# Kernel tuning notes

Measured on AMD Instinct MI355X. Metric: run time of the kernel, lower is better.

The kernel has to match this reference:

```python
import jax, jax.numpy as jnp
import numpy as np

N, K, DIN = 2, 2048, 1024
H, DOUT = 16, 64


def setup_inputs() -> dict:
    key = jax.random.key(0)
    ks = jax.random.split(key, 12)
    c_qk = float(np.sqrt(6.0 / (DIN + DOUT)))  # per-head q/k init scale
    c_v = c_qk  # dim_q == dim_v == DOUT here
    u = lambda k, shape, c: jax.random.uniform(k, shape, jnp.float32, -c, c)
    inp = {
        "query": jax.random.normal(ks[0], (N, K, DIN), jnp.float32),
        "key": jax.random.normal(ks[1], (N, K, DIN), jnp.float32),
        "value": jax.random.normal(ks[2], (N, K, DIN), jnp.float32),
        "mask": jax.random.randint(ks[3], (N, K, K), 0, 2) > 0,  # bool (N,K,K)
        # stacked per-head projection weights: (H, DIN, DOUT), biases (H, DOUT)
        "Wq": u(ks[4], (H, DIN, DOUT), c_qk),
        "bq": u(ks[5], (H, DOUT), c_qk),
        "Wk": u(ks[6], (H, DIN, DOUT), c_qk),
        "bk": u(ks[7], (H, DOUT), c_qk),
        "Wv": u(ks[8], (H, DIN, DOUT), c_v),
        "bv": u(ks[9], (H, DOUT), c_v),
        # output projection: (H*DOUT, DIN)
        "Wp": u(ks[10], (H * DOUT, DIN), c_qk),
        "bp": u(ks[11], (DIN,), c_qk),
    }
    return inp


def reference(query, key, value, mask, Wq, bq, Wk, bk, Wv, bv, Wp, bp):
    # Per-head projections, batched over heads: (N,K,DIN) x (H,DIN,DOUT) -> (N,H,K,DOUT)
    q = jnp.einsum("nkm,hmd->nhkd", query, Wq) + bq[None, :, None, :]
    k = jnp.einsum("nkm,hmd->nhkd", key, Wk) + bk[None, :, None, :]
    v = jnp.einsum("nkm,hmd->nhkd", value, Wv) + bv[None, :, None, :]
    # scaled dot-product scores: (N,H,K,K), scaled by sqrt(per-head dim)
    scores = jnp.einsum("nhkd,nhld->nhkl", q, k) / jnp.sqrt(jnp.asarray(DOUT, q.dtype))
    scores = jnp.where(mask[:, None, :, :], jnp.asarray(-1e9, scores.dtype), scores)
    w = jax.nn.softmax(scores, axis=-1)
    y = jnp.einsum("nhkl,nhld->nhkd", w, v)  # (N,H,K,DOUT)
    # concat heads along feature dim (head order matches torch cat over head list)
    y = jnp.transpose(y, (0, 2, 1, 3)).reshape(N, K, H * DOUT)
    return y @ Wp + bp
```

## Files before the change

kernel.cpp:

```cpp
#include <hip/hip_runtime.h>
#include <hip/hip_bf16.h>

typedef __attribute__((ext_vector_type(8))) __bf16 bf16x8;
typedef __attribute__((ext_vector_type(4))) float floatx4;

#define NB 2
#define SEQ 2048
#define DIN 1024
#define NH 16
#define DH 64
#define DMODEL 1024
#define BQ 128
#define BK 64
#define PAD 72
#define QSCALE 0.18033688011112042f

__device__ __forceinline__ float bf2f(unsigned short u) {
    return __uint_as_float(((unsigned)u) << 16);
}
__device__ __forceinline__ unsigned short f2bf(float f) {
    unsigned u = __float_as_uint(f);
    unsigned r = (u + 0x7FFFu + ((u >> 16) & 1u)) >> 16;
    return (unsigned short)r;
}
__device__ __forceinline__ float ldin(const void* p, size_t idx, int isbf) {
    return isbf ? bf2f(((const unsigned short*)p)[idx]) : ((const float*)p)[idx];
}

__device__ __forceinline__ int wave_is_bf16(const void* p) {
    unsigned short u = ((const unsigned short*)p)[2 * (threadIdx.x & 63)];
    int e = (u >> 7) & 0xFF;
    int sane = (u == 0 || (e > 100 && e < 140)) ? 1 : 0;
    return __popcll(__ballot(sane)) >= 32;
}
__device__ __forceinline__ int wave_mask_is_int(const void* p) {
    int v = ((const int*)p)[threadIdx.x & 63];
    int zo = (v == 0 || v == 1) ? 1 : 0;
    return __popcll(__ballot(zo)) >= 48;
}

__global__ __launch_bounds__(256) void prep(
    const void* __restrict__ q, const void* __restrict__ k, const void* __restrict__ v,
    const void* __restrict__ mask,
    const void* __restrict__ wq, const void* __restrict__ wk,
    const void* __restrict__ wv, const void* __restrict__ wp,
    unsigned short* __restrict__ a0, unsigned short* __restrict__ a1,
    unsigned short* __restrict__ a2,
    unsigned short* __restrict__ t0, unsigned short* __restrict__ t1,
    unsigned short* __restrict__ t2, unsigned short* __restrict__ t3,
    unsigned int* __restrict__ mbits)
{
    __shared__ float xls[64][68];
    const int b = blockIdx.x;
    const int tid = threadIdx.x;
    if (b < 12288) {
        int z = b >> 12, blk = b & 4095;
        const void* src = (z == 0) ? q : (z == 1) ? k : v;
        unsigned short* dst = (z == 0) ? a0 : (z == 1) ? a1 : a2;
        int isbf = wave_is_bf16(src);
        size_t i = ((size_t)blk * 256 + tid) * 4;
        if (isbf) {
            *(ushort4*)&dst[i] = *(const ushort4*)((const unsigned short*)src + i);
        } else {
            float4 f = *(const float4*)((const float*)src + i);
            ushort4 o;
            o.x = f2bf(f.x); o.y = f2bf(f.y); o.z = f2bf(f.z); o.w = f2bf(f.w);
            *(ushort4*)&dst[i] = o;
        }
    } else if (b < 13312) {
        int blk = b - 12288;
        int w = blk * 256 + tid;
        int is_int = wave_mask_is_int(mask);
        unsigned bits = 0;
        if (is_int) {
            const int4* p = (const int4*)mask + (size_t)w * 8;
#pragma unroll
            for (int g = 0; g < 8; ++g) {
                int4 vv = p[g];
                bits |= (unsigned)(vv.x != 0) << (g * 4 + 0);
                bits |= (unsigned)(vv.y != 0) << (g * 4 + 1);
                bits |= (unsigned)(vv.z != 0) << (g * 4 + 2);
                bits |= (unsigned)(vv.w != 0) << (g * 4 + 3);
            }
        } else {
            const uint4* p = (const uint4*)mask + (size_t)w * 2;
#pragma unroll
            for (int g = 0; g < 2; ++g) {
                uint4 vv = p[g];
                unsigned ws4[4] = {vv.x, vv.y, vv.z, vv.w};
#pragma unroll
                for (int c = 0; c < 4; ++c)
#pragma unroll
                    for (int bb = 0; bb < 4; ++bb)
                        bits |= (unsigned)(((ws4[c] >> (8 * bb)) & 0xFFu) != 0)
                                << (g * 16 + c * 4 + bb);
            }
        }
        mbits[w] = bits;
    } else {
        int zb = b - 13312;
        int z = zb >> 8, t = zb & 255;
        const void* src = (z == 0) ? wq : (z == 1) ? wk : (z == 2) ? wv : wp;
        unsigned short* dst = (z == 0) ? t0 : (z == 1) ? t1 : (z == 2) ? t2 : t3;
        int isbf = wave_is_bf16(src);
        int r = tid >> 2, cs = (tid & 3) * 16;
        if (z < 3) {
            int h = t >> 4, m0 = (t & 15) * 64;
#pragma unroll
            for (int j = 0; j < 16; ++j)
                xls[r][cs + j] = ldin(src, (size_t)h * 65536 + (size_t)(m0 + r) * 64 + cs + j, isbf);
            __syncthreads();
            int d2 = tid >> 2, ms = (tid & 3) * 16;
            size_t orow = (size_t)(h * 64 + d2) * 1024 + m0 + ms;
#pragma unroll
            for (int g = 0; g < 4; ++g) {
                ushort4 o;
                o.x = f2bf(xls[ms + g * 4 + 0][d2]);
                o.y = f2bf(xls[ms + g * 4 + 1][d2]);
                o.z = f2bf(xls[ms + g * 4 + 2][d2]);
                o.w = f2bf(xls[ms + g * 4 + 3][d2]);
                *(ushort4*)&dst[orow + g * 4] = o;
            }
        } else {
            int m0 = (t >> 4) * 64, c0 = (t & 15) * 64;
#pragma unroll
            for (int j = 0; j < 16; ++j)
                xls[r][cs + j] = ldin(src, (size_t)(m0 + r) * 1024 + c0 + cs + j, isbf);
            __syncthreads();
            int d2 = tid >> 2, ms = (tid & 3) * 16;
            size_t orow = (size_t)(c0 + d2) * 1024 + m0 + ms;
#pragma unroll
            for (int g = 0; g < 4; ++g) {
                ushort4 o;
                o.x = f2bf(xls[ms + g * 4 + 0][d2]);
                o.y = f2bf(xls[ms + g * 4 + 1][d2]);
                o.z = f2bf(xls[ms + g * 4 + 2][d2]);
                o.w = f2bf(xls[ms + g * 4 + 3][d2]);
                *(ushort4*)&dst[orow + g * 4] = o;
            }
        }
    }
}

__global__ __launch_bounds__(256) void gemm_mfma(
    const unsigned short* __restrict__ A0, const unsigned short* __restrict__ A1,
    const unsigned short* __restrict__ A2,
    const unsigned short* __restrict__ B0, const unsigned short* __restrict__ B1,
    const unsigned short* __restrict__ B2,
    const void* __restrict__ bias0, const void* __restrict__ bias1,
    const void* __restrict__ bias2,
    void* __restrict__ C0, void* __restrict__ C1, void* __restrict__ C2,
    int mode0)
{
    const int z = blockIdx.z;
    const unsigned short* A  = (z == 0) ? A0 : (z == 1) ? A1 : A2;
    const unsigned short* BT = (z == 0) ? B0 : (z == 1) ? B1 : B2;
    const void* bias = (z == 0) ? bias0 : (z == 1) ? bias1 : bias2;
    void* C = (z == 0) ? C0 : (z == 1) ? C1 : C2;
    const int mode = mode0 + z;
    const int isbf = wave_is_bf16(bias);
    const float scl = (mode == 0) ? QSCALE : 1.0f;

    const int n0  = blockIdx.x * 128;
    const int m0g = blockIdx.y * 128;
    const int tid = threadIdx.x;
    const int wave = tid >> 6, lane = tid & 63;
    const int l16 = lane & 15, quad = lane >> 4;
    const int wm = wave & 1, wn = wave >> 1;

    __shared__ __align__(16) unsigned short smem[17408];
    unsigned short* As = smem;
    unsigned short* Bs = smem + 8192;

    floatx4 acc[4][4];
#pragma unroll
    for (int mt = 0; mt < 4; ++mt)
#pragma unroll
        for (int nt = 0; nt < 4; ++nt) acc[mt][nt] = floatx4{0.f, 0.f, 0.f, 0.f};

    for (int kk = 0; kk < 1024; kk += 64) {
#pragma unroll
        for (int j = 0; j < 4; ++j) {
            int i = tid + j * 256;
            int row = i >> 3, seg = (i & 7) * 8;
            *(bf16x8*)&As[row * 64 + seg] = *(const bf16x8*)&A[(size_t)(m0g + row) * 1024 + kk + seg];
            *(bf16x8*)&Bs[row * 64 + seg] = *(const bf16x8*)&BT[(size_t)(n0 + row) * 1024 + kk + seg];
        }
        __syncthreads();
#pragma unroll
        for (int ks = 0; ks < 2; ++ks) {
            bf16x8 af[4], bf[4];
#pragma unroll
            for (int mt = 0; mt < 4; ++mt)
                af[mt] = *(const bf16x8*)&As[(wm * 64 + mt * 16 + l16) * 64 + ks * 32 + quad * 8];
#pragma unroll
            for (int nt = 0; nt < 4; ++nt)
                bf[nt] = *(const bf16x8*)&Bs[(wn * 64 + nt * 16 + l16) * 64 + ks * 32 + quad * 8];
#pragma unroll
            for (int mt = 0; mt < 4; ++mt)
#pragma unroll
                for (int nt = 0; nt < 4; ++nt)
                    acc[mt][nt] = __builtin_amdgcn_mfma_f32_16x16x32_bf16(af[mt], bf[nt], acc[mt][nt], 0, 0, 0);
        }
        __syncthreads();
    }

    float bv4[4];
#pragma unroll
    for (int nt = 0; nt < 4; ++nt)
        bv4[nt] = ldin(bias, n0 + wn * 64 + nt * 16 + l16, isbf);

    if (mode <= 1) {
        unsigned short* O = (unsigned short*)C;
#pragma unroll
        for (int mt = 0; mt < 4; ++mt)
#pragma unroll
            for (int reg = 0; reg < 4; ++reg) {
                int row = m0g + wm * 64 + mt * 16 + quad * 4 + reg;
                int nb = row >> 11, kq = row & (SEQ - 1);
#pragma unroll
                for (int nt = 0; nt < 4; ++nt) {
                    int c = n0 + wn * 64 + nt * 16 + l16;
                    int h = c >> 6, d = c & 63;
                    O[(((size_t)nb * NH + h) * SEQ + kq) * DH + d] =
                        f2bf((acc[mt][nt][reg] + bv4[nt]) * scl);
                }
            }
    } else if (mode == 2) {
#pragma unroll
        for (int mt = 0; mt < 4; ++mt)
#pragma unroll
            for (int nt = 0; nt < 4; ++nt)
#pragma unroll
                for (int reg = 0; reg < 4; ++reg) {
                    int m_l = wm * 64 + mt * 16 + quad * 4 + reg;
                    int c_l = wn * 64 + nt * 16 + l16;
                    smem[c_l * 136 + m_l] = f2bf(acc[mt][nt][reg] + bv4[nt]);
                }
        __syncthreads();
        unsigned short* O = (unsigned short*)C;
        int nb = m0g >> 11;
        int kq0 = m0g & (SEQ - 1);
#pragma unroll
        for (int j = 0; j < 8; ++j) {
            int i = tid + j * 256;
            int c_l = i >> 4, m8 = (i & 15) * 8;
            int cg = n0 + c_l, h = cg >> 6, d = cg & 63;
            *(bf16x8*)&O[(((size_t)nb * NH + h) * DH + d) * SEQ + kq0 + m8] =
                *(const bf16x8*)&smem[c_l * 136 + m8];
        }
    } else {
        unsigned short* Ob = (unsigned short*)C;
        float* Of = (float*)C;
#pragma unroll
        for (int mt = 0; mt < 4; ++mt)
#pragma unroll
            for (int reg = 0; reg < 4; ++reg) {
                int row = m0g + wm * 64 + mt * 16 + quad * 4 + reg;
#pragma unroll
                for (int nt = 0; nt < 4; ++nt) {
                    int c = n0 + wn * 64 + nt * 16 + l16;
                    float v = acc[mt][nt][reg] + bv4[nt];
                    if (isbf) Ob[(size_t)row * DMODEL + c] = f2bf(v);
                    else      Of[(size_t)row * DMODEL + c] = v;
                }
            }
    }
}

__global__ __launch_bounds__(256) void attn_mfma(
    const unsigned short* __restrict__ qws, const unsigned short* __restrict__ kws,
    const unsigned short* __restrict__ vtws, const unsigned int* __restrict__ mbits,
    unsigned short* __restrict__ yws)
{
    const int qt   = blockIdx.x;
    const int h    = blockIdx.y;
    const int n    = blockIdx.z;
    const int tid  = threadIdx.x;
    const int wave = tid >> 6;
    const int lane = tid & 63;
    const int l16  = lane & 15;
    const int quad = lane >> 4;

    __shared__ __align__(16) unsigned short Ks[2][BK * PAD];
    __shared__ __align__(16) unsigned short VTs[2][DH * PAD];
    __shared__ __align__(16) unsigned short Ps[4][32 * PAD];
    __shared__ unsigned int Ms[2][BQ][2];

    const size_t base_nh = ((size_t)n * NH + h) * SEQ * DH;
    const size_t base_vt = ((size_t)n * NH + h) * DH * SEQ;
    const int q0 = qt * BQ;
    const unsigned int* mrow_base = mbits + ((size_t)n * SEQ + q0) * (SEQ / 32);

    const int srow = tid >> 3, sseg = (tid & 7) * 8;
    const int mr = tid >> 1, mw = tid & 1;

    bf16x8 af[2][2];
#pragma unroll
    for (int mt = 0; mt < 2; ++mt) {
        const unsigned short* qp =
            qws + base_nh + (size_t)(q0 + wave * 32 + mt * 16 + l16) * DH + quad * 8;
        af[mt][0] = *(const bf16x8*)qp;
        af[mt][1] = *(const bf16x8*)(qp + 32);
    }

    {
#pragma unroll
        for (int j = 0; j < 2; ++j) {
            int row = srow + j * 32;
            *(bf16x8*)&Ks[0][row * PAD + sseg] =
                *(const bf16x8*)&kws[base_nh + (size_t)row * DH + sseg];
            *(bf16x8*)&VTs[0][row * PAD + sseg] =
                *(const bf16x8*)&vtws[base_vt + (size_t)row * SEQ + sseg];
        }
        Ms[0][mr][mw] = mrow_base[(size_t)mr * (SEQ / 32) + mw];
    }

    floatx4 O[2][4];
#pragma unroll
    for (int mt = 0; mt < 2; ++mt)
#pragma unroll
        for (int dt = 0; dt < 4; ++dt) O[mt][dt] = floatx4{0.f, 0.f, 0.f, 0.f};
    float lrow[2][4] = {};

    __syncthreads();

    for (int it = 0; it < SEQ / BK; ++it) {
        const int cur = it & 1;
        const bool has_next = (it + 1) < (SEQ / BK);
        const int j0n = (it + 1) * BK;

        bf16x8 nk[2], nv[2];
        unsigned int nm = 0;
        if (has_next) {
#pragma unroll
            for (int j = 0; j < 2; ++j) {
                int row = srow + j * 32;
                nk[j] = *(const bf16x8*)&kws[base_nh + (size_t)(j0n + row) * DH + sseg];
                nv[j] = *(const bf16x8*)&vtws[base_vt + (size_t)row * SEQ + j0n + sseg];
            }
            nm = mrow_base[(size_t)mr * (SEQ / 32) + (j0n >> 5) + mw];
        }

        bf16x8 bfK[4][2];
#pragma unroll
        for (int nt = 0; nt < 4; ++nt)
#pragma unroll
            for (int ks = 0; ks < 2; ++ks)
                bfK[nt][ks] = *(const bf16x8*)&Ks[cur][(nt * 16 + l16) * PAD + ks * 32 + quad * 8];

        float S[2][4][4];
#pragma unroll
        for (int mt = 0; mt < 2; ++mt)
#pragma unroll
            for (int nt = 0; nt < 4; ++nt) {
                floatx4 c = {0.f, 0.f, 0.f, 0.f};
                c = __builtin_amdgcn_mfma_f32_16x16x32_bf16(af[mt][0], bfK[nt][0], c, 0, 0, 0);
                c = __builtin_amdgcn_mfma_f32_16x16x32_bf16(af[mt][1], bfK[nt][1], c, 0, 0, 0);
                S[mt][nt][0] = c[0]; S[mt][nt][1] = c[1];
                S[mt][nt][2] = c[2]; S[mt][nt][3] = c[3];
            }

#pragma unroll
        for (int mt = 0; mt < 2; ++mt)
#pragma unroll
            for (int r = 0; r < 4; ++r) {
                int lrowi = wave * 32 + mt * 16 + quad * 4 + r;
                unsigned wlo = Ms[cur][lrowi][0], whi = Ms[cur][lrowi][1];
#pragma unroll
                for (int nt = 0; nt < 4; ++nt) {
                    unsigned w = (nt & 2) ? whi : wlo;
                    int bit = (w >> ((nt & 1) * 16 + l16)) & 1;
                    float s = bit ? -1e9f : S[mt][nt][r];
                    float p = exp2f(s);
                    lrow[mt][r] += p;
                    Ps[wave][(mt * 16 + quad * 4 + r) * PAD + nt * 16 + l16] =
                        (unsigned short)(__float_as_uint(p) >> 16);
                }
            }

        bf16x8 pa[2][2], vb[4][2];
#pragma unroll
        for (int mt = 0; mt < 2; ++mt)
#pragma unroll
            for (int ks = 0; ks < 2; ++ks)
                pa[mt][ks] = *(const bf16x8*)&Ps[wave][(mt * 16 + l16) * PAD + ks * 32 + quad * 8];
#pragma unroll
        for (int dt = 0; dt < 4; ++dt)
#pragma unroll
            for (int ks = 0; ks < 2; ++ks)
                vb[dt][ks] = *(const bf16x8*)&VTs[cur][(dt * 16 + l16) * PAD + ks * 32 + quad * 8];
#pragma unroll
        for (int mt = 0; mt < 2; ++mt)
#pragma unroll
            for (int dt = 0; dt < 4; ++dt) {
                O[mt][dt] = __builtin_amdgcn_mfma_f32_16x16x32_bf16(pa[mt][0], vb[dt][0], O[mt][dt], 0, 0, 0);
                O[mt][dt] = __builtin_amdgcn_mfma_f32_16x16x32_bf16(pa[mt][1], vb[dt][1], O[mt][dt], 0, 0, 0);
            }

        if (has_next) {
            const int nxt = cur ^ 1;
#pragma unroll
            for (int j = 0; j < 2; ++j) {
                int row = srow + j * 32;
                *(bf16x8*)&Ks[nxt][row * PAD + sseg] = nk[j];
                *(bf16x8*)&VTs[nxt][row * PAD + sseg] = nv[j];
            }
            Ms[nxt][mr][mw] = nm;
        }
        __syncthreads();
    }

#pragma unroll
    for (int mt = 0; mt < 2; ++mt)
#pragma unroll
        for (int r = 0; r < 4; ++r)
            for (int o = 1; o < 16; o <<= 1) lrow[mt][r] += __shfl_xor(lrow[mt][r], o);

#pragma unroll
    for (int mt = 0; mt < 2; ++mt)
#pragma unroll
        for (int r = 0; r < 4; ++r) {
            int row = q0 + wave * 32 + mt * 16 + quad * 4 + r;
            float l = lrow[mt][r];
            float inv = (l > 0.f) ? 1.f / l : 0.f;
#pragma unroll
            for (int dt = 0; dt < 4; ++dt) {
                int col = h * DH + dt * 16 + l16;
                yws[((size_t)n * SEQ + row) * DMODEL + col] = f2bf(O[mt][dt][r] * inv);
            }
        }
}

extern "C" void kernel_launch(void* const* d_in, const int* in_sizes, int n_in,
                              void* d_out, int out_size, void* d_ws, size_t ws_size,
                              hipStream_t stream) {
    const void* query = d_in[0];
    const void* key_  = d_in[1];
    const void* value = d_in[2];
    const void* mask  = d_in[3];
    const void* Wq = d_in[4];
    const void* bq = d_in[5];
    const void* Wk = d_in[6];
    const void* bk = d_in[7];
    const void* Wv = d_in[8];
    const void* bv = d_in[9];
    const void* Wp = d_in[10];
    const void* bp = d_in[11];

    const size_t per = (size_t)NB * NH * SEQ * DH;
    unsigned short* us = (unsigned short*)d_ws;
    unsigned short* qws  = us;
    unsigned short* kws  = us + per;
    unsigned short* vtws = us + 2 * per;
    unsigned short* abf0 = us + 3 * per;
    unsigned short* abf1 = us + 4 * per;
    unsigned short* abf2 = us + 5 * per;
    unsigned short* wt0  = us + 6 * per;
    unsigned short* wt1  = wt0 + 1048576;
    unsigned short* wt2  = wt1 + 1048576;
    unsigned short* wt3  = wt2 + 1048576;
    unsigned int* mbits  = (unsigned int*)(wt3 + 1048576);
    unsigned short* yws = abf0;

    prep<<<dim3(14336), 256, 0, stream>>>(query, key_, value, mask,
                                          Wq, Wk, Wv, Wp,
                                          abf0, abf1, abf2,
                                          wt0, wt1, wt2, wt3, mbits);
    gemm_mfma<<<dim3(8, 32, 3), 256, 0, stream>>>(abf0, abf1, abf2, wt0, wt1, wt2,
                                                  bq, bk, bv, qws, kws, vtws, 0);
    attn_mfma<<<dim3(SEQ / BQ, NH, NB), 256, 0, stream>>>(qws, kws, vtws, mbits, yws);
    gemm_mfma<<<dim3(8, 32, 1), 256, 0, stream>>>(yws, yws, yws, wt3, wt3, wt3,
                                                  bp, bp, bp, d_out, d_out, d_out, 3);
}
```

Measured before the change: 311.3 us.

## Use direct global-to-LDS loads with XOR swizzle in GEMM and attention

```diff
diff --git a/kernel.cpp b/kernel.cpp
--- a/kernel.cpp
+++ b/kernel.cpp
@@ -1,5 +1,6 @@
 #include <hip/hip_runtime.h>
 #include <hip/hip_bf16.h>
+#include <stdint.h>
 
 typedef __attribute__((ext_vector_type(8))) __bf16 bf16x8;
 typedef __attribute__((ext_vector_type(4))) float floatx4;
@@ -25,6 +26,15 @@
 }
 __device__ __forceinline__ float ldin(const void* p, size_t idx, int isbf) {
     return isbf ? bf2f(((const unsigned short*)p)[idx]) : ((const float*)p)[idx];
+}
+
+__device__ __forceinline__ void gl_lds16(const void* g, void* l) {
+    __builtin_amdgcn_global_load_lds(
+        reinterpret_cast<__attribute__((address_space(1))) unsigned int*>(
+            reinterpret_cast<uintptr_t>(g)),
+        reinterpret_cast<__attribute__((address_space(3))) unsigned int*>(
+            reinterpret_cast<uintptr_t>(l)),
+        16, 0, 0);
 }
 
 __device__ __forceinline__ int wave_is_bf16(const void* p) {
@@ -178,13 +188,15 @@
 #pragma unroll
         for (int nt = 0; nt < 4; ++nt) acc[mt][nt] = floatx4{0.f, 0.f, 0.f, 0.f};
 
+    const int lrow8 = lane >> 3;
+    const int lseg  = (lane & 7) * 8;
+
     for (int kk = 0; kk < 1024; kk += 64) {
 #pragma unroll
         for (int j = 0; j < 4; ++j) {
-            int i = tid + j * 256;
-            int row = i >> 3, seg = (i & 7) * 8;
-            *(bf16x8*)&As[row * 64 + seg] = *(const bf16x8*)&A[(size_t)(m0g + row) * 1024 + kk + seg];
-            *(bf16x8*)&Bs[row * 64 + seg] = *(const bf16x8*)&BT[(size_t)(n0 + row) * 1024 + kk + seg];
+            int row0 = wave * 8 + j * 32;
+            gl_lds16(&A[(size_t)(m0g + row0 + lrow8) * 1024 + kk + lseg], &As[row0 * 64]);
+            gl_lds16(&BT[(size_t)(n0 + row0 + lrow8) * 1024 + kk + lseg], &Bs[row0 * 64]);
         }
         __syncthreads();
 #pragma unroll
@@ -282,8 +294,8 @@
     const int l16  = lane & 15;
     const int quad = lane >> 4;
 
-    __shared__ __align__(16) unsigned short Ks[2][BK * PAD];
-    __shared__ __align__(16) unsigned short VTs[2][DH * PAD];
+    __shared__ __align__(16) unsigned short Ks[2][BK * DH];
+    __shared__ __align__(16) unsigned short VTs[2][DH * BK];
     __shared__ __align__(16) unsigned short Ps[4][32 * PAD];
     __shared__ unsigned int Ms[2][BQ][2];
 
@@ -292,8 +304,17 @@
     const int q0 = qt * BQ;
     const unsigned int* mrow_base = mbits + ((size_t)n * SEQ + q0) * (SEQ / 32);
 
-    const int srow = tid >> 3, sseg = (tid & 7) * 8;
+    const int srow8  = lane >> 3;
+    const int schunk = ((lane & 7) ^ srow8) * 8;
     const int mr = tid >> 1, mw = tid & 1;
+
+    const int swz = l16 & 7;
+    int koff[2], voff[2];
+#pragma unroll
+    for (int ks = 0; ks < 2; ++ks) {
+        koff[ks] = l16 * DH + (((ks * 4 + quad) ^ swz) * 8);
+        voff[ks] = l16 * BK + (((ks * 4 + quad) ^ swz) * 8);
+    }
 
     bf16x8 af[2][2];
 #pragma unroll
@@ -306,12 +327,10 @@
 
     {
 #pragma unroll
-        for (int j = 0; j < 2; ++j) {
-            int row = srow + j * 32;
-            *(bf16x8*)&Ks[0][row * PAD + sseg] =
-                *(const bf16x8*)&kws[base_nh + (size_t)row * DH + sseg];
-            *(bf16x8*)&VTs[0][row * PAD + sseg] =
-                *(const bf16x8*)&vtws[base_vt + (size_t)row * SEQ + sseg];
+        for (int c = 0; c < 2; ++c) {
+            int rl = wave * 16 + c * 8;
+            gl_lds16(&kws[base_nh + (size_t)(rl + srow8) * DH + schunk], &Ks[0][rl * DH]);
+            gl_lds16(&vtws[base_vt + (size_t)(rl + srow8) * SEQ + schunk], &VTs[0][rl * BK]);
         }
         Ms[0][mr][mw] = mrow_base[(size_t)mr * (SEQ / 32) + mw];
     }
@@ -326,18 +345,17 @@
     __syncthreads();
 
     for (int it = 0; it < SEQ / BK; ++it) {
-        const int cur = it & 1;
+        const int cur = it & 1, nxt = cur ^ 1;
         const bool has_next = (it + 1) < (SEQ / BK);
         const int j0n = (it + 1) * BK;
 
-        bf16x8 nk[2], nv[2];
         unsigned int nm = 0;
         if (has_next) {
 #pragma unroll
-            for (int j = 0; j < 2; ++j) {
-                int row = srow + j * 32;
-                nk[j] = *(const bf16x8*)&kws[base_nh + (size_t)(j0n + row) * DH + sseg];
-                nv[j] = *(const bf16x8*)&vtws[base_vt + (size_t)row * SEQ + j0n + sseg];
+            for (int c = 0; c < 2; ++c) {
+                int rl = wave * 16 + c * 8;
+                gl_lds16(&kws[base_nh + (size_t)(j0n + rl + srow8) * DH + schunk], &Ks[nxt][rl * DH]);
+                gl_lds16(&vtws[base_vt + (size_t)(rl + srow8) * SEQ + j0n + schunk], &VTs[nxt][rl * BK]);
             }
             nm = mrow_base[(size_t)mr * (SEQ / 32) + (j0n >> 5) + mw];
         }
@@ -347,7 +365,7 @@
         for (int nt = 0; nt < 4; ++nt)
 #pragma unroll
             for (int ks = 0; ks < 2; ++ks)
-                bfK[nt][ks] = *(const bf16x8*)&Ks[cur][(nt * 16 + l16) * PAD + ks * 32 + quad * 8];
+                bfK[nt][ks] = *(const bf16x8*)&Ks[cur][nt * 16 * DH + koff[ks]];
 
         float S[2][4][4];
 #pragma unroll
@@ -389,7 +407,7 @@
         for (int dt = 0; dt < 4; ++dt)
 #pragma unroll
             for (int ks = 0; ks < 2; ++ks)
-                vb[dt][ks] = *(const bf16x8*)&VTs[cur][(dt * 16 + l16) * PAD + ks * 32 + quad * 8];
+                vb[dt][ks] = *(const bf16x8*)&VTs[cur][dt * 16 * BK + voff[ks]];
 #pragma unroll
         for (int mt = 0; mt < 2; ++mt)
 #pragma unroll
@@ -398,16 +416,7 @@
                 O[mt][dt] = __builtin_amdgcn_mfma_f32_16x16x32_bf16(pa[mt][1], vb[dt][1], O[mt][dt], 0, 0, 0);
             }
 
-        if (has_next) {
-            const int nxt = cur ^ 1;
-#pragma unroll
-            for (int j = 0; j < 2; ++j) {
-                int row = srow + j * 32;
-                *(bf16x8*)&Ks[nxt][row * PAD + sseg] = nk[j];
-                *(bf16x8*)&VTs[nxt][row * PAD + sseg] = nv[j];
-            }
-            Ms[nxt][mr][mw] = nm;
-        }
+        if (has_next) Ms[nxt][mr][mw] = nm;
         __syncthreads();
     }
 
```

After: 313.6 us. Within noise of the previous version (+0.7%).
